# Performance work log

Measured on AMD Instinct MI355X. Metric: run time of the kernel, lower is better.

Reference implementation:

```python
import jax, jax.numpy as jnp
import numpy as np
from jax import lax

B, T, V, E, H, K = 64, 512, 30000, 256, 256, 9


def setup_inputs() -> dict:
    key = jax.random.key(0)
    ks = jax.random.split(key, 15)
    s = 0.08
    return {
        "word_inputs": jax.random.randint(ks[0], (B, T), 0, V),
        "word_seq_lengths": jax.random.randint(ks[1], (B,), 1, T + 1),
        "seq_token_label": jax.random.randint(ks[2], (B, T), 0, K),
        "word_vec": jax.random.normal(ks[3], (V, E), jnp.float32) * s,
        "W_ih_f": jax.random.normal(ks[4], (4 * H, E), jnp.float32) * s,
        "W_hh_f": jax.random.normal(ks[5], (4 * H, H), jnp.float32) * s,
        "b_f": jax.random.normal(ks[6], (4 * H,), jnp.float32) * s,
        "W_ih_b": jax.random.normal(ks[7], (4 * H, E), jnp.float32) * s,
        "W_hh_b": jax.random.normal(ks[8], (4 * H, H), jnp.float32) * s,
        "b_b": jax.random.normal(ks[9], (4 * H,), jnp.float32) * s,
        "W_out": jax.random.normal(ks[10], (K, 2 * H), jnp.float32) * s,
        "b_out": jax.random.normal(ks[11], (K,), jnp.float32) * s,
        "start_trans": jax.random.normal(ks[12], (K,), jnp.float32) * s,
        "end_trans": jax.random.normal(ks[13], (K,), jnp.float32) * s,
        "trans": jax.random.normal(ks[14], (K, K), jnp.float32) * s,
    }


def _lstm_dir(x, W_ih, W_hh, b):
    # x: [B,T,E] -> h: [B,T,H]; torch gate order (i, f, g, o)
    gx = jnp.einsum('bte,ge->btg', x, W_ih) + b  # input projection hoisted out of scan
    h0 = jnp.zeros((x.shape[0], W_hh.shape[1]), x.dtype)

    def step(carry, g_t):
        h, c = carry
        g = g_t + h @ W_hh.T
        i, f, gg, o = jnp.split(g, 4, axis=-1)
        c = jax.nn.sigmoid(f) * c + jax.nn.sigmoid(i) * jnp.tanh(gg)
        h = jax.nn.sigmoid(o) * jnp.tanh(c)
        return (h, c), h

    _, hs = lax.scan(step, (h0, h0), jnp.swapaxes(gx, 0, 1))
    return jnp.swapaxes(hs, 0, 1)


def reference(word_inputs, word_seq_lengths, seq_token_label, word_vec,
              W_ih_f, W_hh_f, b_f, W_ih_b, W_hh_b, b_b,
              W_out, b_out, start_trans, end_trans, trans):
    t_idx = jnp.arange(T)
    mask = t_idx[None, :] < word_seq_lengths[:, None]  # [B,T] bool (pack_padded semantics)
    # index map that reverses the valid prefix of each sequence (involution)
    rev_idx = jnp.where(mask, word_seq_lengths[:, None] - 1 - t_idx[None, :], t_idx[None, :])

    emb = word_vec[word_inputs]  # [B,T,E]
    h_fwd = _lstm_dir(emb, W_ih_f, W_hh_f, b_f)
    emb_rev = jnp.take_along_axis(emb, rev_idx[:, :, None], axis=1)
    h_bwd = jnp.take_along_axis(_lstm_dir(emb_rev, W_ih_b, W_hh_b, b_b), rev_idx[:, :, None], axis=1)
    feats = jnp.concatenate([h_fwd, h_bwd], axis=-1) * mask[:, :, None]  # [B,T,2H]
    emissions = feats @ W_out.T + b_out  # [B,T,K]

    mf = mask.astype(emissions.dtype)
    # ---- CRF numerator (score of gold path) ----
    emit_sc = jnp.take_along_axis(emissions, seq_token_label[:, :, None], 2)[:, :, 0]  # [B,T]
    num = start_trans[seq_token_label[:, 0]] + emit_sc[:, 0]
    trans_sc = trans[seq_token_label[:, :-1], seq_token_label[:, 1:]]  # [B,T-1]
    num = num + jnp.sum((trans_sc + emit_sc[:, 1:]) * mf[:, 1:], axis=1)
    last_tags = jnp.take_along_axis(seq_token_label, (word_seq_lengths - 1)[:, None], 1)[:, 0]
    num = num + end_trans[last_tags]

    # ---- CRF log-partition (alpha recursion) ----
    em_t = jnp.swapaxes(emissions[:, 1:], 0, 1)  # [T-1,B,K]
    mk_t = jnp.swapaxes(mask[:, 1:], 0, 1)       # [T-1,B]
    score0 = start_trans[None, :] + emissions[:, 0]  # [B,K]

    def alpha_step(score, inp):
        e_t, m_t = inp
        nxt = jax.nn.logsumexp(score[:, :, None] + trans[None], axis=1) + e_t
        return jnp.where(m_t[:, None], nxt, score), None

    scoreZ, _ = lax.scan(alpha_step, score0, (em_t, mk_t))
    denom = jax.nn.logsumexp(scoreZ + end_trans[None, :], axis=1)
    ner_loss = -jnp.mean(num - denom)  # reduction='mean' over batch, negated

    # ---- Viterbi decode ----
    def vit_step(score, inp):
        e_t, m_t = inp
        tot = score[:, :, None] + trans[None]  # [B,K,K]
        best_prev = jnp.argmax(tot, axis=1)    # [B,K]
        nxt = jnp.max(tot, axis=1) + e_t
        return jnp.where(m_t[:, None], nxt, score), best_prev

    scoreV, hist = lax.scan(vit_step, score0, (em_t, mk_t))  # hist [T-1,B,K]
    best_last = jnp.argmax(scoreV + end_trans[None, :], axis=1)  # [B]

    def back_step(cur, inp):
        h_t, m_t = inp
        new = jnp.take_along_axis(h_t, cur[:, None], 1)[:, 0]
        cur = jnp.where(m_t, new, cur)
        return cur, cur

    _, preds_rev = lax.scan(back_step, best_last, (hist[::-1], mk_t[::-1]))  # [T-1,B]
    preds = jnp.concatenate([jnp.swapaxes(preds_rev[::-1], 0, 1), best_last[:, None]], axis=1)  # [B,T]
    preds = jnp.where(mask, preds, 0)

    return ner_loss, preds, feats
```

## Files before the change

### kernel.cpp

```cpp
#include <hip/hip_runtime.h>
#include <hip/hip_bf16.h>
#include <math.h>

#ifndef __has_builtin
#define __has_builtin(x) 0
#endif

typedef unsigned int uint;
typedef unsigned short ushort;
typedef _Float16 half2_t __attribute__((ext_vector_type(2)));

#define PREG 96
#define WREG_UINTS (PREG * 2 * 512)
#define WLDS_UINTS (16 * 512 * 4)

__device__ __forceinline__ float sigm(float x) {
    return __fdividef(1.0f, 1.0f + __expf(-x));
}
__device__ __forceinline__ float tanh_fast(float x) {
    float sg = __fdividef(1.0f, 1.0f + __expf(-2.0f * x));
    return sg + sg - 1.0f;
}
__device__ __forceinline__ float dot2f(uint w, uint h, float acc) {
#if __has_builtin(__builtin_amdgcn_fdot2)
    return __builtin_amdgcn_fdot2(__builtin_bit_cast(half2_t, w),
                                  __builtin_bit_cast(half2_t, h), acc, false);
#else
    half2_t a = __builtin_bit_cast(half2_t, w);
    half2_t b = __builtin_bit_cast(half2_t, h);
    return acc + (float)a.x * (float)b.x + (float)a.y * (float)b.y;
#endif
}
__device__ __forceinline__ uint packh2(float a, float b) {
    ushort u0 = __builtin_bit_cast(ushort, (_Float16)a);
    ushort u1 = __builtin_bit_cast(ushort, (_Float16)b);
    return (uint)u0 | ((uint)u1 << 16);
}

#define R96(X) \
  X(0) X(1) X(2) X(3) X(4) X(5) X(6) X(7) \
  X(8) X(9) X(10) X(11) X(12) X(13) X(14) X(15) \
  X(16) X(17) X(18) X(19) X(20) X(21) X(22) X(23) \
  X(24) X(25) X(26) X(27) X(28) X(29) X(30) X(31) \
  X(32) X(33) X(34) X(35) X(36) X(37) X(38) X(39) \
  X(40) X(41) X(42) X(43) X(44) X(45) X(46) X(47) \
  X(48) X(49) X(50) X(51) X(52) X(53) X(54) X(55) \
  X(56) X(57) X(58) X(59) X(60) X(61) X(62) X(63) \
  X(64) X(65) X(66) X(67) X(68) X(69) X(70) X(71) \
  X(72) X(73) X(74) X(75) X(76) X(77) X(78) X(79) \
  X(80) X(81) X(82) X(83) X(84) X(85) X(86) X(87) \
  X(88) X(89) X(90) X(91) X(92) X(93) X(94) X(95)

#define R16(X) \
  X(0) X(1) X(2) X(3) X(4) X(5) X(6) X(7) \
  X(8) X(9) X(10) X(11) X(12) X(13) X(14) X(15)

#define WDECL(m) uint wA##m, wB##m;
#define WLOAD(m) wA##m = wreg[(2 * (m)) * 512 + tid]; \
                 wB##m = wreg[(2 * (m) + 1) * 512 + tid];
#define WSTEP(m) { \
    uint hp = (uint)__builtin_amdgcn_readlane((int)((m) < 64 ? r0 : r1), (m) & 63); \
    aA = dot2f(wA##m, hp, aA); \
    aB = dot2f(wB##m, hp, aB); }
#define LSTEP(i) { \
    uint4 w4 = reinterpret_cast<const uint4*>(lw)[((i) << 9) + tid]; \
    uint hp0 = (uint)__builtin_amdgcn_readlane((int)r1, 32 + 2 * (i)); \
    uint hp1 = (uint)__builtin_amdgcn_readlane((int)r1, 33 + 2 * (i)); \
    aA = dot2f(w4.x, hp0, aA); \
    aB = dot2f(w4.y, hp0, aB); \
    aA = dot2f(w4.z, hp1, aA); \
    aB = dot2f(w4.w, hp1, aB); }

__global__ __launch_bounds__(256) void zero_kernel(float* __restrict__ out,
                                                   const int* __restrict__ lens) {
    int bid = blockIdx.x;
    if (bid < 65536) {
        int g = bid * 256 + threadIdx.x;
        int row = g >> 9;
        int t = row & 511;
        int b = row >> 9;
        if (t >= lens[b]) out[32769 + g] = 0.0f;
    } else if (bid < 65536 + 128) {
        int p = (bid - 65536) * 256 + threadIdx.x;
        out[1 + p] = 0.0f;
    } else if (threadIdx.x == 0) {
        out[0] = 0.0f;
    }
}

__global__ __launch_bounds__(256) void pack_kernel(const float* __restrict__ WF,
                                                   const float* __restrict__ WB,
                                                   uint* __restrict__ wregF,
                                                   uint* __restrict__ wregB,
                                                   uint* __restrict__ wldsF,
                                                   uint* __restrict__ wldsB) {
    int id = blockIdx.x * 256 + threadIdx.x;
    const float* W = WF; uint* wr = wregF; uint* wl = wldsF;
    if (id >= 131072) { id -= 131072; W = WB; wr = wregB; wl = wldsB; }
    int m, x, tl, dst_lds = 0, id2 = 0;
    if (id < WREG_UINTS) {
        m = id >> 10;
        int r = id & 1023;
        x = r >> 9;
        tl = r & 511;
    } else {
        id2 = id - WREG_UINTS;
        int c = id2 & 3;
        int u = id2 >> 2;
        tl = u & 511;
        int g = u >> 9;
        m = PREG + 2 * g + (c >> 1);
        x = c & 1;
        dst_lds = 1;
    }
    int j = tl >> 1, s = tl & 1;
    int q = (s << 1) + x;
    const float* row = W + ((size_t)((q << 8) + j) << 8);
    uint pk = packh2(row[2 * m], row[2 * m + 1]);
    if (dst_lds) wl[id2] = pk;
    else         wr[((m << 1) + x) * 512 + tl] = pk;
}

__global__ __launch_bounds__(256) void wih_pack_kernel(const float* __restrict__ WihF,
                                                       const float* __restrict__ WihB,
                                                       uint* __restrict__ w16F,
                                                       uint* __restrict__ w16B) {
    int id = blockIdx.x * 256 + threadIdx.x;
    const float* W = WihF; uint* dst = w16F;
    if (id >= 131072) { id -= 131072; W = WihB; dst = w16B; }
    int col = id >> 7;
    int p = id & 127;
    int perm = ((col & 3) << 8) + (col >> 2);
    const float* row = W + ((size_t)perm << 8);
    dst[(col << 7) + p] = packh2(row[2 * p], row[2 * p + 1]);
}

__global__ __launch_bounds__(256) void gemm_gx_kernel(const int* __restrict__ widx,
                                                      const int* __restrict__ lens,
                                                      const float* __restrict__ wvec,
                                                      const uint* __restrict__ wih16,
                                                      const float* __restrict__ bias,
                                                      _Float16* __restrict__ gx) {
    int row0 = blockIdx.x * 64;
    int b = row0 >> 9;
    int t0 = row0 & 511;
    if (t0 >= lens[b]) return;
    int n0 = blockIdx.y * 64;

    __shared__ __align__(16) uint As[16][68];
    __shared__ __align__(16) uint Bs[16][68];
    __shared__ int aoff[64];

    int tid = threadIdx.x;
    if (tid < 64) aoff[tid] = widx[row0 + tid] << 8;
    __syncthreads();

    float acc[4][4] = {};
    int tn = tid & 15, tm = tid >> 4;

    for (int k0p = 0; k0p < 128; k0p += 16) {
#pragma unroll
        for (int p = 0; p < 4; ++p) {
            int lin = p * 256 + tid;
            int kp = lin & 15, m = lin >> 4;
            const float2 av = *reinterpret_cast<const float2*>(
                &wvec[aoff[m] + ((k0p + kp) << 1)]);
            As[kp][m] = packh2(av.x, av.y);
            Bs[kp][m] = wih16[((n0 + m) << 7) + k0p + kp];
        }
        __syncthreads();
#pragma unroll
        for (int kp = 0; kp < 16; ++kp) {
            uint4 a4 = *reinterpret_cast<const uint4*>(&As[kp][tm * 4]);
            uint4 b4 = *reinterpret_cast<const uint4*>(&Bs[kp][tn * 4]);
            uint am[4] = {a4.x, a4.y, a4.z, a4.w};
            uint bn[4] = {b4.x, b4.y, b4.z, b4.w};
#pragma unroll
            for (int i = 0; i < 4; ++i)
#pragma unroll
                for (int j = 0; j < 4; ++j) acc[i][j] = dot2f(am[i], bn[j], acc[i][j]);
        }
        __syncthreads();
    }

#pragma unroll
    for (int i = 0; i < 4; ++i) {
        int row = row0 + tm * 4 + i;
        ushort u[4];
#pragma unroll
        for (int j = 0; j < 4; ++j) {
            int col = n0 + tn * 4 + j;
            int perm = ((col & 3) << 8) + (col >> 2);
            u[j] = __builtin_bit_cast(ushort, (_Float16)(acc[i][j] + bias[perm]));
        }
        uint2 st;
        st.x = (uint)u[0] | ((uint)u[1] << 16);
        st.y = (uint)u[2] | ((uint)u[3] << 16);
        *reinterpret_cast<uint2*>(&gx[row * 1024 + n0 + tn * 4]) = st;
    }
}

__global__ __launch_bounds__(512, 2) void lstm_kernel(const _Float16* __restrict__ gx0,
                                                      const _Float16* __restrict__ gx1,
                                                      const uint* __restrict__ wreg0,
                                                      const uint* __restrict__ wreg1,
                                                      const uint* __restrict__ wlds0,
                                                      const uint* __restrict__ wlds1,
                                                      const int* __restrict__ lens,
                                                      float* __restrict__ feats) {
    int dir = blockIdx.x & 1;
    int b = blockIdx.x >> 1;
    const uint* gxu = reinterpret_cast<const uint*>(dir ? gx1 : gx0) + ((size_t)(b << 9) << 9);
    const uint* wreg = dir ? wreg1 : wreg0;
    const uint* wlds = dir ? wlds1 : wlds0;
    int len = lens[b];
    int tid = threadIdx.x;
    int lane = tid & 63;
    int sg = tid & 1;

    __shared__ __align__(16) uint lw[WLDS_UINTS];
    __shared__ __align__(16) uint hpair[2][128];

    for (int i = tid; i < WLDS_UINTS; i += 512) lw[i] = wlds[i];

    R96(WDECL)
    R96(WLOAD)
    __syncthreads();

    float c = 0.0f;
    uint r0 = 0, r1 = 0;
    int pp = 0;

    int t0i = dir ? (len - 1) : 0;
    uint g = gxu[(t0i << 9) + tid];

    for (int tp = 0; tp < len; ++tp) {
        int t = dir ? (len - 1 - tp) : tp;
        int tnn = dir ? (len - 2 - tp) : (tp + 1);
        tnn = tnn < 0 ? 0 : (tnn >= len ? len - 1 : tnn);
        uint gnext = gxu[(tnn << 9) + tid];

        half2_t gv = __builtin_bit_cast(half2_t, g);
        float aA = (float)gv.x;
        float aB = (float)gv.y;

        R96(WSTEP)
        R16(LSTEP)

        float y = sg ? aA + aA : aA;
        float sgm = __fdividef(1.0f, 1.0f + __expf(-y));
        float pA = sg ? sgm + sgm - 1.0f : sgm;
        float pB = sigm(aB);

        float oA = __shfl_xor(pA, 1);
        float oB = __shfl_xor(pB, 1);
        float si = sg ? oA : pA;
        float sf = sg ? oB : pB;
        float tg = sg ? pA : oA;
        float so = sg ? pB : oB;

        c = sf * c + si * tg;
        float h = so * tanh_fast(c);

        if (!sg) {
            reinterpret_cast<ushort*>(hpair[pp])[tid >> 1] =
                __builtin_bit_cast(ushort, (_Float16)h);
            feats[(size_t)(((b << 9) + t)) * 512 + (dir << 8) + (tid >> 1)] = h;
        }
        __syncthreads();
        r0 = hpair[pp][lane];
        r1 = hpair[pp][64 + lane];
        pp ^= 1;
        g = gnext;
    }
}

__global__ __launch_bounds__(64) void emis_kernel(const float* __restrict__ feats,
                                                  const float* __restrict__ Wout,
                                                  const float* __restrict__ bout,
                                                  const int* __restrict__ lens,
                                                  float* __restrict__ emis) {
    int r = blockIdx.x;
    int b = r >> 9, t = r & 511;
    if (t >= lens[b]) return;
    int lane = threadIdx.x;
    const float* fr = feats + (size_t)r * 512;
    float f[8];
#pragma unroll
    for (int i = 0; i < 8; ++i) f[i] = fr[i * 64 + lane];
#pragma unroll
    for (int k = 0; k < 9; ++k) {
        float p = 0.0f;
#pragma unroll
        for (int i = 0; i < 8; ++i) p = fmaf(f[i], Wout[k * 512 + i * 64 + lane], p);
#pragma unroll
        for (int off = 32; off; off >>= 1) p += __shfl_down(p, off);
        if (lane == 0) emis[r * 9 + k] = p + bout[k];
    }
}

__global__ __launch_bounds__(64) void crf_kernel(const float* __restrict__ emis,
                                                 const int* __restrict__ lens,
                                                 const int* __restrict__ labels,
                                                 const float* __restrict__ start_trans,
                                                 const float* __restrict__ end_trans,
                                                 const float* __restrict__ trans,
                                                 float* __restrict__ out) {
    int b = blockIdx.x;
    int len = lens[b];
    int lane = threadIdx.x;
    __shared__ float alpha[9], vit[9];
    __shared__ unsigned char hist[512 * 9];
    const float* eb = emis + b * 512 * 9;
    const int* lb = labels + b * 512;

    float tr[9];
    if (lane < 9) {
#pragma unroll
        for (int i = 0; i < 9; ++i) tr[i] = trans[i * 9 + lane];
        float s0 = start_trans[lane] + eb[lane];
        alpha[lane] = s0;
        vit[lane] = s0;
    }
    __syncthreads();

    for (int t = 1; t < len; ++t) {
        float na = 0.0f, nv = 0.0f;
        if (lane < 9) {
            float e = eb[t * 9 + lane];
            float a[9];
#pragma unroll
            for (int i = 0; i < 9; ++i) a[i] = alpha[i] + tr[i];
            float m = a[0];
#pragma unroll
            for (int i = 1; i < 9; ++i) m = fmaxf(m, a[i]);
            float s = 0.0f;
#pragma unroll
            for (int i = 0; i < 9; ++i) s += __expf(a[i] - m);
            na = m + __logf(s) + e;
            float bv = vit[0] + tr[0];
            int bi = 0;
#pragma unroll
            for (int i = 1; i < 9; ++i) {
                float x = vit[i] + tr[i];
                if (x > bv) { bv = x; bi = i; }
            }
            nv = bv + e;
            hist[t * 9 + lane] = (unsigned char)bi;
        }
        __syncthreads();
        if (lane < 9) { alpha[lane] = na; vit[lane] = nv; }
        __syncthreads();
    }

    float part = 0.0f;
    for (int t = 1 + lane; t < len; t += 64) {
        int yp = lb[t - 1], y = lb[t];
        part += trans[yp * 9 + y] + eb[t * 9 + y];
    }
#pragma unroll
    for (int off = 32; off; off >>= 1) part += __shfl_down(part, off);

    if (lane == 0) {
        int y0 = lb[0];
        float num = start_trans[y0] + eb[y0] + part + end_trans[lb[len - 1]];
        float m = alpha[0] + end_trans[0];
        for (int j = 1; j < 9; ++j) m = fmaxf(m, alpha[j] + end_trans[j]);
        float s = 0.0f;
        for (int j = 0; j < 9; ++j) s += __expf(alpha[j] + end_trans[j] - m);
        float denom = m + __logf(s);
        atomicAdd(out, (denom - num) * (1.0f / 64.0f));

        float bm = vit[0] + end_trans[0];
        int cur = 0;
        for (int j = 1; j < 9; ++j) {
            float x = vit[j] + end_trans[j];
            if (x > bm) { bm = x; cur = j; }
        }
        float* preds = out + 1 + b * 512;
        preds[len - 1] = (float)cur;
        for (int t = len - 1; t >= 1; --t) {
            cur = hist[t * 9 + cur];
            preds[t - 1] = (float)cur;
        }
    }
}

extern "C" void kernel_launch(void* const* d_in, const int* in_sizes, int n_in,
                              void* d_out, int out_size, void* d_ws, size_t ws_size,
                              hipStream_t stream) {
    const int* widx = (const int*)d_in[0];
    const int* lens = (const int*)d_in[1];
    const int* labels = (const int*)d_in[2];
    const float* wvec = (const float*)d_in[3];
    const float* WihF = (const float*)d_in[4];
    const float* WhhF = (const float*)d_in[5];
    const float* bF = (const float*)d_in[6];
    const float* WihB = (const float*)d_in[7];
    const float* WhhB = (const float*)d_in[8];
    const float* bB = (const float*)d_in[9];
    const float* Wout = (const float*)d_in[10];
    const float* bout = (const float*)d_in[11];
    const float* start_trans = (const float*)d_in[12];
    const float* end_trans = (const float*)d_in[13];
    const float* trans9 = (const float*)d_in[14];
    float* out = (float*)d_out;
    char* ws = (char*)d_ws;

    _Float16* gxF = (_Float16*)(ws);
    _Float16* gxB = (_Float16*)(ws + 67108864);
    uint* wregF   = (uint*)(ws + 134217728);
    uint* wregB   = (uint*)(ws + 134610944);
    uint* wldsF   = (uint*)(ws + 135004160);
    uint* wldsB   = (uint*)(ws + 135135232);
    uint* wih16F  = (uint*)(ws + 135266304);
    uint* wih16B  = (uint*)(ws + 135790592);
    float* emis   = (float*)(ws + 135266304);
    (void)in_sizes; (void)n_in; (void)out_size; (void)ws_size;

    float* feats = out + 1 + 32768;

    zero_kernel<<<65665, 256, 0, stream>>>(out, lens);
    pack_kernel<<<1024, 256, 0, stream>>>(WhhF, WhhB, wregF, wregB, wldsF, wldsB);
    wih_pack_kernel<<<1024, 256, 0, stream>>>(WihF, WihB, wih16F, wih16B);

    dim3 ggrid(512, 16);
    gemm_gx_kernel<<<ggrid, 256, 0, stream>>>(widx, lens, wvec, wih16F, bF, gxF);
    gemm_gx_kernel<<<ggrid, 256, 0, stream>>>(widx, lens, wvec, wih16B, bB, gxB);

    lstm_kernel<<<128, 512, 0, stream>>>(gxF, gxB, wregF, wregB, wldsF, wldsB, lens, feats);

    emis_kernel<<<32768, 64, 0, stream>>>(feats, Wout, bout, lens, emis);
    crf_kernel<<<64, 64, 0, stream>>>(emis, lens, labels, start_trans, end_trans, trans9, out);
}
```

Measured before the change: 1.664 ms.

## Compute all four gates per thread in LSTM with 256-thread blocks

The LSTM recurrence now uses one thread per hidden unit, computing all four gates (i,f,g,o) itself, instead of two threads per unit exchanging gate pairs via shuffles. This halves the block size to 256 threads with one wave per EU. Each thread holds 96 uint4 of W_hh in registers (384 VGPRs) and reads the remaining 32 rows from LDS. The weight packing layout changes to match. The aim is to drop the shuffle exchange and halve barrier participants, at the cost of twice the dot-product work per thread and heavy register pressure that may spill.

Result: slower. 2.133 ms (+28.2%).

```diff
diff --git a/kernel.cpp b/kernel.cpp
--- a/kernel.cpp
+++ b/kernel.cpp
@@ -10,9 +10,8 @@
 typedef unsigned short ushort;
 typedef _Float16 half2_t __attribute__((ext_vector_type(2)));
 
-#define PREG 96
-#define WREG_UINTS (PREG * 2 * 512)
-#define WLDS_UINTS (16 * 512 * 4)
+#define WREG_UINTS (96 * 256 * 4)
+#define WLDS_UINTS (32 * 256 * 4)
 
 __device__ __forceinline__ float sigm(float x) {
     return __fdividef(1.0f, 1.0f + __expf(-x));
@@ -51,25 +50,27 @@
   X(80) X(81) X(82) X(83) X(84) X(85) X(86) X(87) \
   X(88) X(89) X(90) X(91) X(92) X(93) X(94) X(95)
 
-#define R16(X) \
+#define R32(X) \
   X(0) X(1) X(2) X(3) X(4) X(5) X(6) X(7) \
-  X(8) X(9) X(10) X(11) X(12) X(13) X(14) X(15)
-
-#define WDECL(m) uint wA##m, wB##m;
-#define WLOAD(m) wA##m = wreg[(2 * (m)) * 512 + tid]; \
-                 wB##m = wreg[(2 * (m) + 1) * 512 + tid];
+  X(8) X(9) X(10) X(11) X(12) X(13) X(14) X(15) \
+  X(16) X(17) X(18) X(19) X(20) X(21) X(22) X(23) \
+  X(24) X(25) X(26) X(27) X(28) X(29) X(30) X(31)
+
+#define WDECL(m) uint4 wv##m;
+#define WLOAD(m) wv##m = wreg4[((m) << 8) + tid];
 #define WSTEP(m) { \
-    uint hp = (uint)__builtin_amdgcn_readlane((int)((m) < 64 ? r0 : r1), (m) & 63); \
-    aA = dot2f(wA##m, hp, aA); \
-    aB = dot2f(wB##m, hp, aB); }
+    uint hpv = (uint)__builtin_amdgcn_readlane((int)((m) < 64 ? r0 : r1), (m) & 63); \
+    aI = dot2f(wv##m.x, hpv, aI); \
+    aF = dot2f(wv##m.y, hpv, aF); \
+    aG = dot2f(wv##m.z, hpv, aG); \
+    aO = dot2f(wv##m.w, hpv, aO); }
 #define LSTEP(i) { \
-    uint4 w4 = reinterpret_cast<const uint4*>(lw)[((i) << 9) + tid]; \
-    uint hp0 = (uint)__builtin_amdgcn_readlane((int)r1, 32 + 2 * (i)); \
-    uint hp1 = (uint)__builtin_amdgcn_readlane((int)r1, 33 + 2 * (i)); \
-    aA = dot2f(w4.x, hp0, aA); \
-    aB = dot2f(w4.y, hp0, aB); \
-    aA = dot2f(w4.z, hp1, aA); \
-    aB = dot2f(w4.w, hp1, aB); }
+    uint4 w4 = lw[((i) << 8) + tid]; \
+    uint hpv = (uint)__builtin_amdgcn_readlane((int)r1, 32 + (i)); \
+    aI = dot2f(w4.x, hpv, aI); \
+    aF = dot2f(w4.y, hpv, aF); \
+    aG = dot2f(w4.z, hpv, aG); \
+    aO = dot2f(w4.w, hpv, aO); }
 
 __global__ __launch_bounds__(256) void zero_kernel(float* __restrict__ out,
                                                    const int* __restrict__ lens) {
@@ -97,28 +98,14 @@
     int id = blockIdx.x * 256 + threadIdx.x;
     const float* W = WF; uint* wr = wregF; uint* wl = wldsF;
     if (id >= 131072) { id -= 131072; W = WB; wr = wregB; wl = wldsB; }
-    int m, x, tl, dst_lds = 0, id2 = 0;
-    if (id < WREG_UINTS) {
-        m = id >> 10;
-        int r = id & 1023;
-        x = r >> 9;
-        tl = r & 511;
-    } else {
-        id2 = id - WREG_UINTS;
-        int c = id2 & 3;
-        int u = id2 >> 2;
-        tl = u & 511;
-        int g = u >> 9;
-        m = PREG + 2 * g + (c >> 1);
-        x = c & 1;
-        dst_lds = 1;
-    }
-    int j = tl >> 1, s = tl & 1;
-    int q = (s << 1) + x;
+    int q = id & 3;
+    int u4 = id >> 2;
+    int j = u4 & 255;
+    int m = u4 >> 8;
     const float* row = W + ((size_t)((q << 8) + j) << 8);
     uint pk = packh2(row[2 * m], row[2 * m + 1]);
-    if (dst_lds) wl[id2] = pk;
-    else         wr[((m << 1) + x) * 512 + tl] = pk;
+    if (m < 96) wr[(((m) << 8) + j) * 4 + q] = pk;
+    else        wl[((((m - 96)) << 8) + j) * 4 + q] = pk;
 }
 
 __global__ __launch_bounds__(256) void wih_pack_kernel(const float* __restrict__ WihF,
@@ -200,28 +187,29 @@
     }
 }
 
-__global__ __launch_bounds__(512, 2) void lstm_kernel(const _Float16* __restrict__ gx0,
-                                                      const _Float16* __restrict__ gx1,
-                                                      const uint* __restrict__ wreg0,
-                                                      const uint* __restrict__ wreg1,
-                                                      const uint* __restrict__ wlds0,
-                                                      const uint* __restrict__ wlds1,
-                                                      const int* __restrict__ lens,
-                                                      float* __restrict__ feats) {
+__global__ __launch_bounds__(256, 1) __attribute__((amdgpu_waves_per_eu(1, 1)))
+void lstm_kernel(const _Float16* __restrict__ gx0,
+                 const _Float16* __restrict__ gx1,
+                 const uint* __restrict__ wreg0,
+                 const uint* __restrict__ wreg1,
+                 const uint* __restrict__ wlds0,
+                 const uint* __restrict__ wlds1,
+                 const int* __restrict__ lens,
+                 float* __restrict__ feats) {
     int dir = blockIdx.x & 1;
     int b = blockIdx.x >> 1;
-    const uint* gxu = reinterpret_cast<const uint*>(dir ? gx1 : gx0) + ((size_t)(b << 9) << 9);
-    const uint* wreg = dir ? wreg1 : wreg0;
-    const uint* wlds = dir ? wlds1 : wlds0;
+    const uint2* gx2 = reinterpret_cast<const uint2*>(dir ? gx1 : gx0) +
+                       ((size_t)b << 17);
+    const uint4* wreg4 = reinterpret_cast<const uint4*>(dir ? wreg1 : wreg0);
+    const uint4* wlds4 = reinterpret_cast<const uint4*>(dir ? wlds1 : wlds0);
     int len = lens[b];
     int tid = threadIdx.x;
     int lane = tid & 63;
-    int sg = tid & 1;
-
-    __shared__ __align__(16) uint lw[WLDS_UINTS];
-    __shared__ __align__(16) uint hpair[2][128];
-
-    for (int i = tid; i < WLDS_UINTS; i += 512) lw[i] = wlds[i];
+
+    __shared__ __align__(16) uint4 lw[32 * 256];
+    __shared__ __align__(16) uint hbuf[2][128];
+
+    for (int i = tid; i < 32 * 256; i += 256) lw[i] = wlds4[i];
 
     R96(WDECL)
     R96(WLOAD)
@@ -232,44 +220,37 @@
     int pp = 0;
 
     int t0i = dir ? (len - 1) : 0;
-    uint g = gxu[(t0i << 9) + tid];
+    uint2 g = gx2[(size_t)t0i * 256 + tid];
 
     for (int tp = 0; tp < len; ++tp) {
         int t = dir ? (len - 1 - tp) : tp;
         int tnn = dir ? (len - 2 - tp) : (tp + 1);
         tnn = tnn < 0 ? 0 : (tnn >= len ? len - 1 : tnn);
-        uint gnext = gxu[(tnn << 9) + tid];
-
-        half2_t gv = __builtin_bit_cast(half2_t, g);
-        float aA = (float)gv.x;
-        float aB = (float)gv.y;
+        uint2 gnext = gx2[(size_t)tnn * 256 + tid];
+
+        half2_t g01 = __builtin_bit_cast(half2_t, g.x);
+        half2_t g23 = __builtin_bit_cast(half2_t, g.y);
+        float aI = (float)g01.x;
+        float aF = (float)g01.y;
+        float aG = (float)g23.x;
+        float aO = (float)g23.y;
 
         R96(WSTEP)
-        R16(LSTEP)
-
-        float y = sg ? aA + aA : aA;
-        float sgm = __fdividef(1.0f, 1.0f + __expf(-y));
-        float pA = sg ? sgm + sgm - 1.0f : sgm;
-        float pB = sigm(aB);
-
-        float oA = __shfl_xor(pA, 1);
-        float oB = __shfl_xor(pB, 1);
-        float si = sg ? oA : pA;
-        float sf = sg ? oB : pB;
-        float tg = sg ? pA : oA;
-        float so = sg ? pB : oB;
-
-        c = sf * c + si * tg;
-        float h = so * tanh_fast(c);
-
-        if (!sg) {
-            reinterpret_cast<ushort*>(hpair[pp])[tid >> 1] =
-                __builtin_bit_cast(ushort, (_Float16)h);
-            feats[(size_t)(((b << 9) + t)) * 512 + (dir << 8) + (tid >> 1)] = h;
-        }
+        R32(LSTEP)
+
+        float iv = sigm(aI);
+        float fv = sigm(aF);
+        float gv = tanh_fast(aG);
+        float ov = sigm(aO);
+        c = fv * c + iv * gv;
+        float h = ov * tanh_fast(c);
+
+        reinterpret_cast<ushort*>(hbuf[pp])[tid] =
+            __builtin_bit_cast(ushort, (_Float16)h);
         __syncthreads();
-        r0 = hpair[pp][lane];
-        r1 = hpair[pp][64 + lane];
+        feats[(size_t)(((b << 9) + t)) * 512 + (dir << 8) + tid] = h;
+        r0 = hbuf[pp][lane];
+        r1 = hbuf[pp][64 + lane];
         pp ^= 1;
         g = gnext;
     }
@@ -428,7 +409,7 @@
     gemm_gx_kernel<<<ggrid, 256, 0, stream>>>(widx, lens, wvec, wih16F, bF, gxF);
     gemm_gx_kernel<<<ggrid, 256, 0, stream>>>(widx, lens, wvec, wih16B, bB, gxB);
 
-    lstm_kernel<<<128, 512, 0, stream>>>(gxF, gxB, wregF, wregB, wldsF, wldsB, lens, feats);
+    lstm_kernel<<<128, 256, 0, stream>>>(gxF, gxB, wregF, wregB, wldsF, wldsB, lens, feats);
 
     emis_kernel<<<32768, 64, 0, stream>>>(feats, Wout, bout, lens, emis);
     crf_kernel<<<64, 64, 0, stream>>>(emis, lens, labels, start_trans, end_trans, trans9, out);
```
